# Kernel tuning notes

Measured on AMD Instinct MI355X. Metric: run time of the kernel, lower is better.

## Reference

```python
import jax, jax.numpy as jnp
import numpy as np

N_FFT = 512
HOP = 128
WIN = 512
Q = 0.1
PCT_WIN = 31
FREQ_WIN = 5
TIME_WIN = 9
STRENGTH = 0.35
THRESH = 1.5
TEMP = 0.15
MIN_MASK = 0.08


def _hann_periodic(n):
    # matches torch.hann_window(n) (periodic)
    return (0.5 * (1.0 - jnp.cos(2.0 * jnp.pi * jnp.arange(n) / n))).astype(jnp.float32)


def _stft(x, window):
    # x: (B, L) -> complex (B, F, T); center=True, reflect pad
    pad = N_FFT // 2
    xp = jnp.pad(x, ((0, 0), (pad, pad)), mode='reflect')
    T = 1 + (xp.shape[-1] - N_FFT) // HOP
    idx = (jnp.arange(T) * HOP)[:, None] + jnp.arange(N_FFT)  # (T, n_fft)
    frames = xp[:, idx] * window  # (B, T, n_fft)
    return jnp.fft.rfft(frames, axis=-1).transpose(0, 2, 1)  # (B, F, T)


def _istft(spec, window, length):
    # spec: (B, F, T) complex -> (B, length)
    frames = jnp.fft.irfft(spec.transpose(0, 2, 1), n=N_FFT, axis=-1) * window  # (B,T,n_fft)
    B, T, _ = frames.shape
    total = N_FFT + HOP * (T - 1)
    idx = ((jnp.arange(T) * HOP)[:, None] + jnp.arange(N_FFT)).ravel()
    out = jnp.zeros((B, total), frames.dtype).at[:, idx].add(frames.reshape(B, -1))
    wsq = jnp.zeros((total,), frames.dtype).at[idx].add(
        jnp.broadcast_to(window ** 2, (T, N_FFT)).ravel())
    out = out / jnp.maximum(wsq, 1e-11)
    pad = N_FFT // 2
    return out[:, pad:pad + length]


def _rolling_quantile(mag):
    # mag: (B, F, T); replicate pad + sliding window of PCT_WIN along time
    p = PCT_WIN // 2
    padded = jnp.pad(mag, ((0, 0), (0, 0), (p, p)), mode='edge')
    T = mag.shape[-1]
    windows = jnp.stack([padded[..., i:i + T] for i in range(PCT_WIN)], axis=-1)  # (B,F,T,W)
    return jnp.quantile(windows, Q, axis=-1)


def _avg_pool(x, k, axis):
    # stride-1 avg pool with zero pad k//2, count_include_pad=True (torch default)
    if k <= 1:
        return x
    p = k // 2
    pads = [(0, 0)] * x.ndim
    pads[axis] = (p, p)
    xp = jnp.pad(x, pads)
    n = x.shape[axis]
    acc = 0.0
    for i in range(k):
        sl = [slice(None)] * x.ndim
        sl[axis] = slice(i, i + n)
        acc = acc + xp[tuple(sl)]
    return acc / k


def setup_inputs() -> dict:
    key = jax.random.key(0)
    k1, k2 = jax.random.split(key)
    B, L = 16, 160000
    noisy = jax.random.normal(k1, (B, L), dtype=jnp.float32)
    enhanced = jax.random.normal(k2, (B, L), dtype=jnp.float32)
    return {"noisy": noisy, "enhanced": enhanced}


def reference(noisy, enhanced):
    length = enhanced.shape[-1]
    window = _hann_periodic(WIN)
    e_spec = _stft(enhanced, window)
    n_spec = _stft(noisy, window)
    e_mag = jnp.maximum(jnp.abs(e_spec), 1e-6)
    n_mag = jnp.maximum(jnp.abs(n_spec), 1e-6)
    # mode == 'sg_input_floor': source is the noisy magnitude
    floor = _rolling_quantile(n_mag)
    floor = _avg_pool(floor, FREQ_WIN, axis=-2)
    floor = _avg_pool(floor, TIME_WIN, axis=-1)
    floor = jnp.maximum(floor, 1e-6)
    mask = jax.nn.sigmoid((e_mag - THRESH * floor) / (TEMP * floor + 1e-6))
    final_mask = MIN_MASK + (1.0 - MIN_MASK) * (1.0 - STRENGTH + STRENGTH * mask)
    phase = e_spec / jnp.maximum(jnp.abs(e_spec), 1e-12)  # unit-phase, = polar(1, angle)
    gated_spec = (e_mag * final_mask).astype(jnp.float32) * phase
    return _istft(gated_spec, window, length)
```

## Files before the change

kernel.cpp:

```cpp
#include <hip/hip_runtime.h>
#include <math.h>

#define BATCH 16
#define LEN   160000
#define NFFT  512
#define HOP   128
#define NT    1251
#define NF    257
#define PADC  256
#define TWO_PI 6.28318530717958647692f
#define P(i) ((i) + ((i) >> 5))
#define FBUF 528
#define GSTR 264

__device__ __forceinline__ int reflect_idx(int j) {
    j = j < 0 ? -j : j;
    j = j >= LEN ? 2*LEN - 2 - j : j;
    return j;
}

__device__ __forceinline__ float hann(int n) {
    return 0.5f - 0.5f * __cosf(TWO_PI * (float)n * (1.0f / 512.0f));
}

struct T4 { float m0, m1, m2, m3; };

__device__ __forceinline__ void ins(T4& a, float v) {
    const float x0 = fminf(a.m0, v);  const float c0 = fmaxf(a.m0, v);
    const float x1 = fminf(a.m1, c0); const float c1 = fmaxf(a.m1, c0);
    const float x2 = fminf(a.m2, c1); const float c2 = fmaxf(a.m2, c1);
    const float x3 = fminf(a.m3, c2);
    a.m0 = x0; a.m1 = x1; a.m2 = x2; a.m3 = x3;
}

__device__ __forceinline__ T4 merge4(const T4& a, const T4& b) {
    const float l0 = fminf(a.m0, b.m3);
    const float l1 = fminf(a.m1, b.m2);
    const float l2 = fminf(a.m2, b.m1);
    const float l3 = fminf(a.m3, b.m0);
    const float t0 = fminf(l0, l2), t2 = fmaxf(l0, l2);
    const float t1 = fminf(l1, l3), t3 = fmaxf(l1, l3);
    T4 r;
    r.m0 = fminf(t0, t1); r.m1 = fmaxf(t0, t1);
    r.m2 = fminf(t2, t3); r.m3 = fmaxf(t2, t3);
    return r;
}

__device__ __forceinline__ T4 sort4(float a, float b, float c, float d) {
    const float x0 = fminf(a, b), x1 = fmaxf(a, b);
    const float x2 = fminf(c, d), x3 = fmaxf(c, d);
    const float y0 = fminf(x0, x2), y2 = fmaxf(x0, x2);
    const float y1 = fminf(x1, x3), y3 = fmaxf(x1, x3);
    T4 r; r.m0 = y0; r.m1 = fminf(y1, y2); r.m2 = fmaxf(y1, y2); r.m3 = y3;
    return r;
}

__device__ __forceinline__ void dft8(float vr[8], float vi[8], float sign) {
    const float K = 0.70710678118654752f;
    float ar=vr[0]+vr[4], ai=vi[0]+vi[4];
    float br=vr[0]-vr[4], bi=vi[0]-vi[4];
    float cr=vr[2]+vr[6], ci=vi[2]+vi[6];
    float dr=vr[2]-vr[6], di=vi[2]-vi[6];
    float er=vr[1]+vr[5], ei=vi[1]+vi[5];
    float fr=vr[1]-vr[5], fi=vi[1]-vi[5];
    float gr=vr[3]+vr[7], gi=vi[3]+vi[7];
    float hr=vr[3]-vr[7], hi=vi[3]-vi[7];
    const float W4dr = -sign*di, W4di = sign*dr;
    const float W4hr = -sign*hi, W4hi = sign*hr;
    const float E0r=ar+cr, E0i=ai+ci, E2r=ar-cr, E2i=ai-ci;
    const float E1r=br+W4dr, E1i=bi+W4di, E3r=br-W4dr, E3i=bi-W4di;
    const float O0r=er+gr, O0i=ei+gi, O2r=er-gr, O2i=ei-gi;
    const float O1r=fr+W4hr, O1i=fi+W4hi, O3r=fr-W4hr, O3i=fi-W4hi;
    const float T1r = K*(O1r - sign*O1i), T1i = K*(O1i + sign*O1r);
    const float T2r = -sign*O2i,          T2i = sign*O2r;
    const float T3r = K*(-O3r - sign*O3i), T3i = K*(-O3i + sign*O3r);
    vr[0]=E0r+O0r; vi[0]=E0i+O0i;  vr[4]=E0r-O0r; vi[4]=E0i-O0i;
    vr[1]=E1r+T1r; vi[1]=E1i+T1i;  vr[5]=E1r-T1r; vi[5]=E1i-T1i;
    vr[2]=E2r+T2r; vi[2]=E2i+T2i;  vr[6]=E2r-T2r; vi[6]=E2i-T2i;
    vr[3]=E3r+T3r; vi[3]=E3i+T3i;  vr[7]=E3r-T3r; vi[7]=E3i-T3i;
}

template<int NS>
__device__ __forceinline__ void fft_pass(float* R, float* I, int j, float sign) {
    float vr[8], vi[8];
    #pragma unroll
    for (int r = 0; r < 8; ++r) { vr[r] = R[P(j + 64*r)]; vi[r] = I[P(j + 64*r)]; }
    const float th = sign * (TWO_PI / (8.0f * (float)NS)) * (float)(j & (NS - 1));
    float w1r, w1i; __sincosf(th, &w1i, &w1r);
    float wr = w1r, wi = w1i;
    #pragma unroll
    for (int r = 1; r < 8; ++r) {
        const float tr = vr[r]*wr - vi[r]*wi;
        vi[r] = vr[r]*wi + vi[r]*wr; vr[r] = tr;
        const float nwr = wr*w1r - wi*w1i;
        wi = wr*w1i + wi*w1r; wr = nwr;
    }
    dft8(vr, vi, sign);
    const int base = ((j / NS) * (8 * NS)) + (j & (NS - 1));
    #pragma unroll
    for (int r = 0; r < 8; ++r) { R[P(base + r*NS)] = vr[r]; I[P(base + r*NS)] = vi[r]; }
}

__global__ __launch_bounds__(256, 4) void stft_kernel(const float* __restrict__ enh,
                                                      const float* __restrict__ noi,
                                                      float2* __restrict__ e_spec,
                                                      float*  __restrict__ n_mag) {
    __shared__ float Ar[4*FBUF], Ai[4*FBUF];
    const int tid = threadIdx.x;
    const int w = tid >> 6, j = tid & 63;
    const int tr_ = blockIdx.x * 4 + w;
    const bool live = tr_ < NT;
    const int t = live ? tr_ : NT - 1;
    const int b = blockIdx.y;
    float* ar = Ar + w*FBUF; float* ai = Ai + w*FBUF;

    {
        const int sbase = t * HOP - PADC;
        const float* __restrict__ pe = enh + b * LEN;
        const float* __restrict__ pn = noi + b * LEN;
        float vr[8], vi[8];
        #pragma unroll
        for (int r = 0; r < 8; ++r) {
            const int n = j + 64*r;
            const int idx = reflect_idx(sbase + n);
            const float wd = hann(n);
            vr[r] = pe[idx] * wd;
            vi[r] = pn[idx] * wd;
        }
        dft8(vr, vi, -1.0f);
        #pragma unroll
        for (int r = 0; r < 8; ++r) { ar[P(8*j + r)] = vr[r]; ai[P(8*j + r)] = vi[r]; }
    }
    fft_pass<8> (ar, ai, j, -1.0f);
    fft_pass<64>(ar, ai, j, -1.0f);

    if (live) {
        const int obase = (b * NT + t) * NF;
        #pragma unroll
        for (int r = 0; r < 5; ++r) {
            const int kk = j + 64*r;
            if (kk > 256) break;
            if (r == 4 && j != 0) break;
            const float zr = ar[P(kk)], zi = ai[P(kk)];
            const int n2 = (512 - kk) & 511;
            const float yr = ar[P(n2)], yi = ai[P(n2)];
            const float er = 0.5f*(zr + yr), ei = 0.5f*(zi - yi);
            const float nr = 0.5f*(zi + yi), ni = 0.5f*(yr - zr);
            e_spec[obase + kk] = make_float2(er, ei);
            n_mag[obase + kk] = fmaxf(sqrtf(nr*nr + ni*ni), 1e-6f);
        }
    }
}

__global__ __launch_bounds__(256) void floor_kernel(const float* __restrict__ n_mag,
                                                    float* __restrict__ floor_) {
    __shared__ float q[24][GSTR];
    __shared__ float fq[24];
    const int tid = threadIdx.x;
    const int t0 = blockIdx.x * 16, b = blockIdx.y;
    const float* __restrict__ pb = n_mag + b * NT * NF;

    {
        float wv[54];
        #pragma unroll
        for (int r = 0; r < 54; ++r) {
            int tr = t0 - 19 + r;
            tr = tr < 0 ? 0 : (tr > NT - 1 ? NT - 1 : tr);
            wv[r] = pb[tr * NF + tid];
        }
        T4 ch[6];
        #pragma unroll
        for (int c = 0; c < 6; ++c)
            ch[c] = merge4(sort4(wv[8*c],   wv[8*c+1], wv[8*c+2], wv[8*c+3]),
                           sort4(wv[8*c+4], wv[8*c+5], wv[8*c+6], wv[8*c+7]));
        #pragma unroll
        for (int k = 0; k < 24; ++k) {
            const int c0 = (k + 7) >> 3;
            T4 m = merge4(merge4(ch[c0], ch[c0+1]), ch[c0+2]);
            #pragma unroll
            for (int jj = k; jj < 8*c0; ++jj) ins(m, wv[jj]);
            #pragma unroll
            for (int jj = 8*c0 + 24; jj < k + 31; ++jj) ins(m, wv[jj]);
            q[k][tid] = m.m3;
        }
    }
    if (tid < 24) {
        const int k = tid;
        T4 m; m.m0 = m.m1 = m.m2 = m.m3 = 3.4e38f;
        for (int dt = -15; dt <= 15; ++dt) {
            int tt = t0 - 4 + k + dt;
            tt = tt < 0 ? 0 : (tt > NT - 1 ? NT - 1 : tt);
            ins(m, pb[tt * NF + 256]);
        }
        q[k][256] = m.m3;
    }
    __syncthreads();

    float fp[24];
    {
        const int f = tid;
        #pragma unroll
        for (int k = 0; k < 24; ++k) {
            float acc = 0.0f;
            #pragma unroll
            for (int df = -2; df <= 2; ++df) {
                const int ff = f + df;
                if (ff >= 0 && ff < NF) acc += q[k][ff];
            }
            fp[k] = acc * (1.0f / 5.0f);
        }
    }
    if (tid < 24) {
        const int k = tid;
        fq[k] = (q[k][254] + q[k][255] + q[k][256]) * (1.0f / 5.0f);
    }
    __syncthreads();

    {
        const int f = tid;
        #pragma unroll
        for (int k = 0; k < 24; ++k) {
            const int tq = t0 - 4 + k;
            fp[k] = (tq >= 0 && tq < NT) ? fp[k] : 0.0f;
        }
        float acc = 0.0f;
        #pragma unroll
        for (int k = 0; k < 9; ++k) acc += fp[k];
        #pragma unroll
        for (int to = 0; to < 16; ++to) {
            const int t = t0 + to;
            if (t < NT)
                floor_[(b * NT + t) * NF + f] = fmaxf(acc * (1.0f / 9.0f), 1e-6f);
            if (to < 15) acc += fp[to + 9] - fp[to];
        }
    }
    if (tid < 16) {
        const int to = tid;
        const int t = t0 + to;
        if (t < NT) {
            float acc = 0.0f;
            #pragma unroll
            for (int k = 0; k < 9; ++k) {
                const int tq = t0 - 4 + to + k;
                acc += (tq >= 0 && tq < NT) ? fq[to + k] : 0.0f;
            }
            floor_[(b * NT + t) * NF + 256] = fmaxf(acc * (1.0f / 9.0f), 1e-6f);
        }
    }
}

__global__ __launch_bounds__(256, 4) void istft_kernel(const float2* __restrict__ g,
                                                       const float* __restrict__ floor_,
                                                       float* __restrict__ frames) {
    __shared__ float gr[8*GSTR], gi[8*GSTR];
    const int tid = threadIdx.x;
    const int w = tid >> 6, j = tid & 63;
    const int t0 = blockIdx.x * 8, b = blockIdx.y;
    const int ta = t0 + 2*w, tb = ta + 1;

    float* g0r = gr + (2*w) * GSTR;      float* g0i = gi + (2*w) * GSTR;
    float* g1r = gr + (2*w + 1) * GSTR;  float* g1i = gi + (2*w + 1) * GSTR;

    for (int e = j; e < 2 * NF; e += 64) {
        const int h = (e >= NF) ? 1 : 0;
        const int kk = e - h * NF;
        const int t = ta + h;
        float grv = 0.0f, giv = 0.0f;
        if (t < NT) {
            const int idx = (b * NT + t) * NF + kk;
            const float fl = floor_[idx];
            const float2 e2 = g[idx];
            const float a = sqrtf(e2.x * e2.x + e2.y * e2.y);
            const float emag = fmaxf(a, 1e-6f);
            const float xarg = (emag - 1.5f * fl) / (0.15f * fl + 1e-6f);
            const float mask = 1.0f / (1.0f + __expf(-xarg));
            const float fm = 0.08f + 0.92f * (0.65f + 0.35f * mask);
            const float scale = emag * fm / fmaxf(a, 1e-12f);
            grv = e2.x * scale; giv = e2.y * scale;
        }
        gr[(2*w + h) * GSTR + kk] = grv;
        gi[(2*w + h) * GSTR + kk] = giv;
    }

    float* ar = g0r;
    float* ai = g0i;

    {
        float vr[8], vi[8];
        #pragma unroll
        for (int r = 0; r < 8; ++r) {
            const int n = j + 64*r;
            float cr, ci;
            if (n <= 256) {
                cr = g0r[n] - g1i[n];
                ci = g0i[n] + g1r[n];
            } else {
                const int m = 512 - n;
                cr = g0r[m] + g1i[m];
                ci = g1r[m] - g0i[m];
            }
            vr[r] = cr; vi[r] = ci;
        }
        dft8(vr, vi, 1.0f);
        #pragma unroll
        for (int r = 0; r < 8; ++r) { ar[P(8*j + r)] = vr[r]; ai[P(8*j + r)] = vi[r]; }
    }
    fft_pass<8> (ar, ai, j, 1.0f);
    fft_pass<64>(ar, ai, j, 1.0f);

    #pragma unroll
    for (int r = 0; r < 8; ++r) {
        const int n = j + 64*r;
        const float wd = hann(n) * (1.0f / 512.0f);
        if (ta < NT) frames[(b * NT + ta) * NFFT + n] = ar[P(n)] * wd;
        if (tb < NT) frames[(b * NT + tb) * NFFT + n] = ai[P(n)] * wd;
    }
}

__global__ __launch_bounds__(256) void ola_kernel(const float* __restrict__ frames,
                                                  float* __restrict__ out) {
    const int j = blockIdx.x * 256 + threadIdx.x;
    if (j >= BATCH * LEN) return;
    const int b = j / LEN;
    const int jj = j - b * LEN;
    const int i = jj + PADC;
    int t_lo = (i >= 384) ? ((i - 384) >> 7) : 0;
    int t_hi = i >> 7; if (t_hi > NT - 1) t_hi = NT - 1;
    if (t_hi - t_lo == 3) {
        const float* __restrict__ fp = frames + (b * NT + t_lo) * NFFT + (i - (t_lo << 7));
        const float acc = fp[0] + fp[384] + fp[768] + fp[1152];
        out[j] = acc * (2.0f / 3.0f);
    } else {
        float acc = 0.0f, wacc = 0.0f;
        for (int t = t_lo; t <= t_hi; ++t) {
            const int n = i - (t << 7);
            const float w = hann(n);
            acc  += frames[(b * NT + t) * NFFT + n];
            wacc += w * w;
        }
        out[j] = acc / fmaxf(wacc, 1e-11f);
    }
}

extern "C" void kernel_launch(void* const* d_in, const int* in_sizes, int n_in,
                              void* d_out, int out_size, void* d_ws, size_t ws_size,
                              hipStream_t stream) {
    const float* noisy    = (const float*)d_in[0];
    const float* enhanced = (const float*)d_in[1];
    float* out = (float*)d_out;

    float* ws = (float*)d_ws;
    float2* e_spec = (float2*)ws;
    float* floor_ = ws + 10288224;
    float* n_mag  = ws + 15432336;
    float* frames = ws + 15432336;

    dim3 blk(256);
    stft_kernel <<<dim3((NT + 3) / 4, BATCH), blk, 0, stream>>>(enhanced, noisy, e_spec, n_mag);
    floor_kernel<<<dim3((NT + 15) / 16, BATCH), blk, 0, stream>>>(n_mag, floor_);
    istft_kernel<<<dim3((NT + 7) / 8, BATCH), blk, 0, stream>>>(e_spec, floor_, frames);
    ola_kernel  <<<dim3((BATCH * LEN + 255) / 256), blk, 0, stream>>>(frames, out);
}
```

Measured before the change: 146.2 us.

## Fuse iSTFT and overlap-add into one kernel using halo frames in LDS

Merges the iSTFT kernel and the overlap-add kernel. Each block now computes 12 frames: 8 owned plus 4 halo frames recomputed from the previous tile. It windows them in shared memory and writes 1024 output samples directly. This removes the global frames buffer round trip and one kernel launch. In exchange, each block does 50% more FFT work and needs more shared memory per block, with 384 threads.

```diff
diff --git a/kernel.cpp b/kernel.cpp
--- a/kernel.cpp
+++ b/kernel.cpp
@@ -249,14 +249,14 @@
     }
 }
 
-__global__ __launch_bounds__(256, 4) void istft_kernel(const float2* __restrict__ g,
-                                                       const float* __restrict__ floor_,
-                                                       float* __restrict__ frames) {
-    __shared__ float gr[8*GSTR], gi[8*GSTR];
+__global__ __launch_bounds__(384) void istft_ola_kernel(const float2* __restrict__ g,
+                                                        const float* __restrict__ floor_,
+                                                        float* __restrict__ out) {
+    __shared__ float gr[12*GSTR], gi[12*GSTR];
     const int tid = threadIdx.x;
     const int w = tid >> 6, j = tid & 63;
     const int t0 = blockIdx.x * 8, b = blockIdx.y;
-    const int ta = t0 + 2*w, tb = ta + 1;
+    const int ta = t0 - 4 + 2*w, tb = ta + 1;
 
     float* g0r = gr + (2*w) * GSTR;      float* g0i = gi + (2*w) * GSTR;
     float* g1r = gr + (2*w + 1) * GSTR;  float* g1i = gi + (2*w + 1) * GSTR;
@@ -266,7 +266,7 @@
         const int kk = e - h * NF;
         const int t = ta + h;
         float grv = 0.0f, giv = 0.0f;
-        if (t < NT) {
+        if (t >= 0 && t < NT) {
             const int idx = (b * NT + t) * NF + kk;
             const float fl = floor_[idx];
             const float2 e2 = g[idx];
@@ -312,33 +312,40 @@
     for (int r = 0; r < 8; ++r) {
         const int n = j + 64*r;
         const float wd = hann(n) * (1.0f / 512.0f);
-        if (ta < NT) frames[(b * NT + ta) * NFFT + n] = ar[P(n)] * wd;
-        if (tb < NT) frames[(b * NT + tb) * NFFT + n] = ai[P(n)] * wd;
-    }
-}
-
-__global__ __launch_bounds__(256) void ola_kernel(const float* __restrict__ frames,
-                                                  float* __restrict__ out) {
-    const int j = blockIdx.x * 256 + threadIdx.x;
-    if (j >= BATCH * LEN) return;
-    const int b = j / LEN;
-    const int jj = j - b * LEN;
-    const int i = jj + PADC;
-    int t_lo = (i >= 384) ? ((i - 384) >> 7) : 0;
-    int t_hi = i >> 7; if (t_hi > NT - 1) t_hi = NT - 1;
-    if (t_hi - t_lo == 3) {
-        const float* __restrict__ fp = frames + (b * NT + t_lo) * NFFT + (i - (t_lo << 7));
-        const float acc = fp[0] + fp[384] + fp[768] + fp[1152];
-        out[j] = acc * (2.0f / 3.0f);
-    } else {
-        float acc = 0.0f, wacc = 0.0f;
-        for (int t = t_lo; t <= t_hi; ++t) {
-            const int n = i - (t << 7);
-            const float w = hann(n);
-            acc  += frames[(b * NT + t) * NFFT + n];
-            wacc += w * w;
-        }
-        out[j] = acc / fmaxf(wacc, 1e-11f);
+        ar[P(n)] *= wd;
+        ai[P(n)] *= wd;
+    }
+    __syncthreads();
+
+    const int ibase = t0 << 7;
+    #pragma unroll
+    for (int s = tid; s < 1024; s += 384) {
+        const int i = ibase + s;
+        const int jj = i - PADC;
+        if (jj < 0 || jj >= LEN) continue;
+        int t_lo = (i >= 384) ? ((i - 384) >> 7) : 0;
+        int t_hi = i >> 7; if (t_hi > NT - 1) t_hi = NT - 1;
+        float acc = 0.0f;
+        if (t_hi - t_lo == 3) {
+            #pragma unroll
+            for (int u = 0; u < 4; ++u) {
+                const int t = t_lo + u;
+                const int ft = t - (t0 - 4);
+                const int n = i - (t << 7);
+                acc += (ft & 1 ? gi : gr)[(ft >> 1) * FBUF + P(n)];
+            }
+            out[b * LEN + jj] = acc * (2.0f / 3.0f);
+        } else {
+            float wacc = 0.0f;
+            for (int t = t_lo; t <= t_hi; ++t) {
+                const int ft = t - (t0 - 4);
+                const int n = i - (t << 7);
+                const float wd = hann(n);
+                acc += (ft & 1 ? gi : gr)[(ft >> 1) * FBUF + P(n)];
+                wacc += wd * wd;
+            }
+            out[b * LEN + jj] = acc / fmaxf(wacc, 1e-11f);
+        }
     }
 }
 
@@ -353,11 +360,8 @@
     float2* e_spec = (float2*)ws;
     float* floor_ = ws + 10288224;
     float* n_mag  = ws + 15432336;
-    float* frames = ws + 15432336;
-
-    dim3 blk(256);
-    stft_kernel <<<dim3((NT + 3) / 4, BATCH), blk, 0, stream>>>(enhanced, noisy, e_spec, n_mag);
-    floor_kernel<<<dim3((NT + 15) / 16, BATCH), blk, 0, stream>>>(n_mag, floor_);
-    istft_kernel<<<dim3((NT + 7) / 8, BATCH), blk, 0, stream>>>(e_spec, floor_, frames);
-    ola_kernel  <<<dim3((BATCH * LEN + 255) / 256), blk, 0, stream>>>(frames, out);
-}
+
+    stft_kernel     <<<dim3((NT + 3) / 4, BATCH), dim3(256), 0, stream>>>(enhanced, noisy, e_spec, n_mag);
+    floor_kernel    <<<dim3((NT + 15) / 16, BATCH), dim3(256), 0, stream>>>(n_mag, floor_);
+    istft_ola_kernel<<<dim3((NT + 7) / 8, BATCH), dim3(384), 0, stream>>>(e_spec, floor_, out);
+}
```

New measurement: 154.2 us. +5.5%, slower.
